# Kernel optimization log

Measured on AMD Instinct MI355X. Metric: run time of the kernel, lower is better.

## Reference

```python
import jax, jax.numpy as jnp
import numpy as np

SIGMA = 1.0
ALPHA = 1.5
EPS = 1e-08
N, D = 8192, 128


def setup_inputs() -> dict:
    key = jax.random.key(0)
    k1, k2 = jax.random.split(key)
    z1 = jax.random.normal(k1, (N, D), dtype=jnp.float32)
    z2 = jax.random.normal(k2, (N, D), dtype=jnp.float32)
    return {"z1": z1, "z2": z2}


def _l2_normalize(x, eps=1e-12):
    # matches F.normalize(x, dim=1): x / max(||x||, eps)
    n = jnp.linalg.norm(x, axis=1, keepdims=True)
    return x / jnp.maximum(n, eps)


def _f_prime(u):
    # KL divergence: f'(u) = log(u + eps) + 1
    return jnp.log(u + EPS) + 1.0


def _f_star(t):
    # KL divergence conjugate: f*(t) = exp(t - 1)
    return jnp.exp(t - 1.0)


def reference(z1, z2):
    z1 = _l2_normalize(z1)
    z2 = _l2_normalize(z2)
    n = z1.shape[0]

    # positive term: ||z1_i - z2_i||^2 per row
    d_pos = jnp.sum((z1 - z2) ** 2, axis=1)                       # (N,)
    g_pos = jnp.exp(-d_pos / (2.0 * SIGMA ** 2))
    s_pos = _f_prime(g_pos)

    # negative term: squared pairwise distances within z1 (N x N)
    sq = jnp.sum(z1 * z1, axis=1)                                  # (N,)
    d2 = sq[:, None] + sq[None, :] - 2.0 * (z1 @ z1.T)             # (N, N)
    d2 = jnp.maximum(d2, 0.0)
    g_neg = jnp.exp(-d2 / (2.0 * SIGMA ** 2))
    s_neg = _f_prime(g_neg)
    star_neg = _f_star(s_neg)

    # masked mean over off-diagonal entries (N*(N-1) of them)
    off_diag = 1.0 - jnp.eye(n, dtype=star_neg.dtype)
    star_mean = jnp.sum(star_neg * off_diag) / (n * (n - 1))

    loss = -jnp.mean(s_pos) + ALPHA * star_mean
    return loss
```

## Files before the change

### kernel.cpp

```cpp
#include <hip/hip_runtime.h>

#define NROWS 8192
#define DIM 128
#define NT 64
#define NPAIRBLK (NT * (NT + 1) / 2)
#define NNORMBLK 2048

typedef _Float16 f16x8 __attribute__((ext_vector_type(8)));
typedef float f32x16 __attribute__((ext_vector_type(16)));

__global__ void fmicl_normalize(const float* __restrict__ z1,
                                const float* __restrict__ z2,
                                float* __restrict__ sq,
                                _Float16* __restrict__ zh,
                                float* __restrict__ spos) {
  const int row = blockIdx.x * 4 + (threadIdx.x >> 6);
  const int lane = threadIdx.x & 63;
  const float* r1 = z1 + (size_t)row * DIM;
  const float* r2 = z2 + (size_t)row * DIM;
  float a0 = r1[lane], a1 = r1[lane + 64];
  float b0 = r2[lane], b1 = r2[lane + 64];
  float s1 = a0 * a0 + a1 * a1;
  float s2 = b0 * b0 + b1 * b1;
#pragma unroll
  for (int off = 32; off; off >>= 1) {
    s1 += __shfl_xor(s1, off);
    s2 += __shfl_xor(s2, off);
  }
  const float inv1 = 1.0f / fmaxf(sqrtf(s1), 1e-12f);
  const float inv2 = 1.0f / fmaxf(sqrtf(s2), 1e-12f);
  const float n1a = a0 * inv1, n1b = a1 * inv1;
  const float n2a = b0 * inv2, n2b = b1 * inv2;
  float sqp = n1a * n1a + n1b * n1b;
  const float da = n1a - n2a, db = n1b - n2b;
  float dp = da * da + db * db;
#pragma unroll
  for (int off = 32; off; off >>= 1) {
    sqp += __shfl_xor(sqp, off);
    dp += __shfl_xor(dp, off);
  }
  zh[(size_t)row * DIM + lane] = (_Float16)n1a;
  zh[(size_t)row * DIM + lane + 64] = (_Float16)n1b;
  if (lane == 0) {
    sq[row] = sqp;
    spos[row] = logf(expf(-0.5f * dp) + 1e-8f) + 1.0f;
  }
}

__global__ __launch_bounds__(512, 4) void fmicl_pairwise(
    const _Float16* __restrict__ zh,
    const float* __restrict__ sq,
    float* __restrict__ pairP) {
  __shared__ _Float16 As[128 * DIM];
  __shared__ _Float16 Bs[128 * DIM];
  __shared__ float wsum[8];

  const int tid = threadIdx.x;
  const int bid = blockIdx.x;

  int rt = (int)(64.5f - sqrtf(64.5f * 64.5f - 2.0f * (float)bid));
  if (rt < 0) rt = 0;
  while (rt > 0 && (rt * NT - (rt * (rt - 1)) / 2) > bid) --rt;
  while (((rt + 1) * NT - ((rt + 1) * rt) / 2) <= bid) ++rt;
  const int ct = rt + (bid - (rt * NT - (rt * (rt - 1)) / 2));

  const int lane = tid & 63;
  const int wid = tid >> 6;
  const int i0 = rt << 7;
  const int j0 = ct << 7;

  const uint4* __restrict__ gA = (const uint4*)(zh + (size_t)i0 * DIM);
  const uint4* __restrict__ gB = (const uint4*)(zh + (size_t)j0 * DIM);
  uint4* sA = (uint4*)As;
  uint4* sB = (uint4*)Bs;
#pragma unroll
  for (int it = 0; it < 4; ++it) {
    const int g = tid + it * 512;
    const int r = g >> 4;
    const int c = g & 15;
    const uint4 va = gA[g];
    const uint4 vb = gB[g];
    const int cs = c ^ (r & 15);
    sA[r * 16 + cs] = va;
    sB[r * 16 + cs] = vb;
  }
  __syncthreads();

  const int l31 = lane & 31;
  const int lhi = lane >> 5;
  const int wm = (wid >> 2) * 64;
  const int wn = (wid & 3) * 32;

  const int ra0 = wm + l31;
  const int ra1 = wm + 32 + l31;
  const int rb = wn + l31;
  f32x16 acc0 = {}, acc1 = {};
#pragma unroll
  for (int ks = 0; ks < 8; ++ks) {
    const int kg = ks * 2 + lhi;
    const uint4 va0 = sA[ra0 * 16 + (kg ^ (ra0 & 15))];
    const uint4 va1 = sA[ra1 * 16 + (kg ^ (ra1 & 15))];
    const uint4 vb = sB[rb * 16 + (kg ^ (rb & 15))];
    const f16x8 bfr = __builtin_bit_cast(f16x8, vb);
    acc0 = __builtin_amdgcn_mfma_f32_32x32x16_f16(
        __builtin_bit_cast(f16x8, va0), bfr, acc0, 0, 0, 0);
    acc1 = __builtin_amdgcn_mfma_f32_32x32x16_f16(
        __builtin_bit_cast(f16x8, va1), bfr, acc1, 0, 0, 0);
  }

  const int gj = j0 + wn + l31;
  const float sj = sq[gj];
  float gsum = 0.0f;
#pragma unroll
  for (int mi = 0; mi < 2; ++mi) {
    const f32x16& acc = mi ? acc1 : acc0;
    const int mbase = wm + mi * 32;
    float4 sqi_q[4];
#pragma unroll
    for (int q = 0; q < 4; ++q)
      sqi_q[q] = *(const float4*)&sq[i0 + mbase + 4 * lhi + 8 * q];
#pragma unroll
    for (int r = 0; r < 16; ++r) {
      const int mloc = (r & 3) + 4 * lhi + 8 * (r >> 2);
      const float si = ((const float*)&sqi_q[r >> 2])[r & 3];
      const float d2 = fmaxf(si + sj - 2.0f * acc[r], 0.0f);
      const float gg = __expf(-0.5f * d2);
      gsum += ((i0 + mbase + mloc) != gj) ? gg : 0.0f;
    }
  }
#pragma unroll
  for (int off = 32; off; off >>= 1) gsum += __shfl_xor(gsum, off);
  if (lane == 0) wsum[wid] = gsum;
  __syncthreads();
  if (tid == 0) {
    const float w = (rt == ct) ? 1.0f : 2.0f;
    float s = 0.0f;
#pragma unroll
    for (int k = 0; k < 8; ++k) s += wsum[k];
    pairP[bid] = w * s;
  }
}

__global__ void fmicl_reduce(const float* __restrict__ pairP,
                             const float* __restrict__ spos,
                             float* __restrict__ out) {
  const int t = threadIdx.x;
  double nsum = (double)pairP[t] + (double)pairP[t + 1024];
  if (t < NPAIRBLK - 2048) nsum += (double)pairP[t + 2048];
  double psum = 0.0;
#pragma unroll
  for (int k = 0; k < 8; ++k) psum += (double)spos[t + 1024 * k];
#pragma unroll
  for (int off = 32; off; off >>= 1) {
    nsum += __shfl_xor(nsum, off);
    psum += __shfl_xor(psum, off);
  }
  __shared__ double ls[2][16];
  const int lane = t & 63;
  const int wid = t >> 6;
  if (lane == 0) {
    ls[0][wid] = nsum;
    ls[1][wid] = psum;
  }
  __syncthreads();
  if (t == 0) {
    double n = 0.0, p = 0.0;
#pragma unroll
    for (int k = 0; k < 16; ++k) {
      n += ls[0][k];
      p += ls[1][k];
    }
    const double pos_mean = p / (double)NROWS;
    const double star_mean = n / ((double)NROWS * (double)(NROWS - 1)) + 1e-8;
    out[0] = (float)(-pos_mean + 1.5 * star_mean);
  }
}

extern "C" void kernel_launch(void* const* d_in, const int* in_sizes, int n_in,
                              void* d_out, int out_size, void* d_ws,
                              size_t ws_size, hipStream_t stream) {
  const float* z1 = (const float*)d_in[0];
  const float* z2 = (const float*)d_in[1];
  float* out = (float*)d_out;
  char* ws = (char*)d_ws;

  float* pairP = (float*)(ws + 0);
  float* spos = (float*)(ws + 16384);
  float* sq = (float*)(ws + 49152);
  _Float16* zh = (_Float16*)(ws + 81920);

  fmicl_normalize<<<NNORMBLK, 256, 0, stream>>>(z1, z2, sq, zh, spos);
  fmicl_pairwise<<<NPAIRBLK, 512, 0, stream>>>(zh, sq, pairP);
  fmicl_reduce<<<1, 1024, 0, stream>>>(pairP, spos, out);
}
```

Baseline: 33.73 us.

## Fuse final reduction into pairwise kernel via last-block atomic ticket

Removes the separate reduce kernel launch: the last pairwise block, found with an atomic counter, does the final double-precision reduction. Normalize pre-reduces the positive term per block and resets the counter. The pairwise kernel moves to 1024 threads with one MFMA tile per wave, loads global memory straight into LDS with global_load_lds, and uses exp2 with folded constants, skipping the diagonal mask except on diagonal warps. This trades a launch and some ALU work for atomic/fence overhead and the removal of the d2 clamp, which can slightly change numerics.

```diff
diff --git a/kernel.cpp b/kernel.cpp
--- a/kernel.cpp
+++ b/kernel.cpp
@@ -4,24 +4,28 @@
 #define DIM 128
 #define NT 64
 #define NPAIRBLK (NT * (NT + 1) / 2)
-#define NNORMBLK 2048
 
 typedef _Float16 f16x8 __attribute__((ext_vector_type(8)));
+typedef _Float16 f16x2 __attribute__((ext_vector_type(2)));
 typedef float f32x16 __attribute__((ext_vector_type(16)));
 
-__global__ void fmicl_normalize(const float* __restrict__ z1,
-                                const float* __restrict__ z2,
-                                float* __restrict__ sq,
-                                _Float16* __restrict__ zh,
-                                float* __restrict__ spos) {
-  const int row = blockIdx.x * 4 + (threadIdx.x >> 6);
+#define KHL2E 0.7213475204444817f
+#define L2E 1.4426950408889634f
+
+#define AS1(p) ((const __attribute__((address_space(1))) void*)(p))
+#define AS3(p) ((__attribute__((address_space(3))) void*)(p))
+
+__global__ __launch_bounds__(1024) void fmicl_normalize(
+    const float* __restrict__ z1, const float* __restrict__ z2,
+    float* __restrict__ sq, _Float16* __restrict__ zh,
+    float* __restrict__ sposB, unsigned int* __restrict__ counter) {
+  const int wid = threadIdx.x >> 6;
   const int lane = threadIdx.x & 63;
-  const float* r1 = z1 + (size_t)row * DIM;
-  const float* r2 = z2 + (size_t)row * DIM;
-  float a0 = r1[lane], a1 = r1[lane + 64];
-  float b0 = r2[lane], b1 = r2[lane + 64];
-  float s1 = a0 * a0 + a1 * a1;
-  float s2 = b0 * b0 + b1 * b1;
+  const int row = blockIdx.x * 16 + wid;
+  const float2 a = ((const float2*)(z1 + (size_t)row * DIM))[lane];
+  const float2 b = ((const float2*)(z2 + (size_t)row * DIM))[lane];
+  float s1 = a.x * a.x + a.y * a.y;
+  float s2 = b.x * b.x + b.y * b.y;
 #pragma unroll
   for (int off = 32; off; off >>= 1) {
     s1 += __shfl_xor(s1, off);
@@ -29,31 +33,43 @@
   }
   const float inv1 = 1.0f / fmaxf(sqrtf(s1), 1e-12f);
   const float inv2 = 1.0f / fmaxf(sqrtf(s2), 1e-12f);
-  const float n1a = a0 * inv1, n1b = a1 * inv1;
-  const float n2a = b0 * inv2, n2b = b1 * inv2;
-  float sqp = n1a * n1a + n1b * n1b;
-  const float da = n1a - n2a, db = n1b - n2b;
-  float dp = da * da + db * db;
+  const float n1x = a.x * inv1, n1y = a.y * inv1;
+  const float n2x = b.x * inv2, n2y = b.y * inv2;
+  float sqp = n1x * n1x + n1y * n1y;
+  const float dx = n1x - n2x, dy = n1y - n2y;
+  float dp = dx * dx + dy * dy;
 #pragma unroll
   for (int off = 32; off; off >>= 1) {
     sqp += __shfl_xor(sqp, off);
     dp += __shfl_xor(dp, off);
   }
-  zh[(size_t)row * DIM + lane] = (_Float16)n1a;
-  zh[(size_t)row * DIM + lane + 64] = (_Float16)n1b;
+  f16x2 h;
+  h.x = (_Float16)n1x;
+  h.y = (_Float16)n1y;
+  *(f16x2*)(zh + (size_t)row * DIM + 2 * lane) = h;
+  __shared__ float sposL[16];
   if (lane == 0) {
     sq[row] = sqp;
-    spos[row] = logf(expf(-0.5f * dp) + 1e-8f) + 1.0f;
+    sposL[wid] = logf(expf(-0.5f * dp) + 1e-8f) + 1.0f;
+  }
+  __syncthreads();
+  if (threadIdx.x == 0) {
+    float s = 0.0f;
+#pragma unroll
+    for (int k = 0; k < 16; ++k) s += sposL[k];
+    sposB[blockIdx.x] = s;
+    if (blockIdx.x == 0) *counter = 0;
   }
 }
 
-__global__ __launch_bounds__(512, 4) void fmicl_pairwise(
-    const _Float16* __restrict__ zh,
-    const float* __restrict__ sq,
-    float* __restrict__ pairP) {
-  __shared__ _Float16 As[128 * DIM];
-  __shared__ _Float16 Bs[128 * DIM];
-  __shared__ float wsum[8];
+__global__ __launch_bounds__(1024, 8) void fmicl_pairwise(
+    const _Float16* __restrict__ zh, const float* __restrict__ sq,
+    float* __restrict__ pairP, const float* __restrict__ sposB,
+    unsigned int* __restrict__ counter, float* __restrict__ out) {
+  __shared__ _Float16 S[256 * DIM];
+  __shared__ float wsum[16];
+  __shared__ double red[32];
+  __shared__ int amLast;
 
   const int tid = threadIdx.x;
   const int bid = blockIdx.x;
@@ -69,63 +85,59 @@
   const int i0 = rt << 7;
   const int j0 = ct << 7;
 
-  const uint4* __restrict__ gA = (const uint4*)(zh + (size_t)i0 * DIM);
-  const uint4* __restrict__ gB = (const uint4*)(zh + (size_t)j0 * DIM);
-  uint4* sA = (uint4*)As;
-  uint4* sB = (uint4*)Bs;
-#pragma unroll
-  for (int it = 0; it < 4; ++it) {
-    const int g = tid + it * 512;
-    const int r = g >> 4;
-    const int c = g & 15;
-    const uint4 va = gA[g];
-    const uint4 vb = gB[g];
-    const int cs = c ^ (r & 15);
-    sA[r * 16 + cs] = va;
-    sB[r * 16 + cs] = vb;
+#pragma unroll
+  for (int t = 0; t < 4; ++t) {
+    const int P = t * 16 + wid;
+    const int R = P * 4 + (lane >> 4);
+    const int csrc = (lane & 15) ^ (R & 15);
+    const _Float16* srow = (R < 128) ? zh + (size_t)(i0 + R) * DIM
+                                     : zh + (size_t)(j0 + R - 128) * DIM;
+    __builtin_amdgcn_global_load_lds(AS1(srow + csrc * 8), AS3(S + P * 512),
+                                     16, 0, 0);
   }
   __syncthreads();
 
   const int l31 = lane & 31;
   const int lhi = lane >> 5;
-  const int wm = (wid >> 2) * 64;
+  const int wm = (wid >> 2) * 32;
   const int wn = (wid & 3) * 32;
-
-  const int ra0 = wm + l31;
-  const int ra1 = wm + 32 + l31;
-  const int rb = wn + l31;
-  f32x16 acc0 = {}, acc1 = {};
+  const uint4* S4 = (const uint4*)S;
+  const int ra = wm + l31;
+  const int rb = 128 + wn + l31;
+  f32x16 acc = {};
 #pragma unroll
   for (int ks = 0; ks < 8; ++ks) {
     const int kg = ks * 2 + lhi;
-    const uint4 va0 = sA[ra0 * 16 + (kg ^ (ra0 & 15))];
-    const uint4 va1 = sA[ra1 * 16 + (kg ^ (ra1 & 15))];
-    const uint4 vb = sB[rb * 16 + (kg ^ (rb & 15))];
-    const f16x8 bfr = __builtin_bit_cast(f16x8, vb);
-    acc0 = __builtin_amdgcn_mfma_f32_32x32x16_f16(
-        __builtin_bit_cast(f16x8, va0), bfr, acc0, 0, 0, 0);
-    acc1 = __builtin_amdgcn_mfma_f32_32x32x16_f16(
-        __builtin_bit_cast(f16x8, va1), bfr, acc1, 0, 0, 0);
+    const uint4 va = S4[ra * 16 + (kg ^ (ra & 15))];
+    const uint4 vb = S4[rb * 16 + (kg ^ (rb & 15))];
+    acc = __builtin_amdgcn_mfma_f32_32x32x16_f16(
+        __builtin_bit_cast(f16x8, va), __builtin_bit_cast(f16x8, vb), acc,
+        0, 0, 0);
   }
 
   const int gj = j0 + wn + l31;
-  const float sj = sq[gj];
+  const float ksj = KHL2E * sq[gj];
+  float4 sqi[4];
+#pragma unroll
+  for (int q = 0; q < 4; ++q)
+    sqi[q] = *(const float4*)&sq[i0 + wm + 4 * lhi + 8 * q];
   float gsum = 0.0f;
-#pragma unroll
-  for (int mi = 0; mi < 2; ++mi) {
-    const f32x16& acc = mi ? acc1 : acc0;
-    const int mbase = wm + mi * 32;
-    float4 sqi_q[4];
-#pragma unroll
-    for (int q = 0; q < 4; ++q)
-      sqi_q[q] = *(const float4*)&sq[i0 + mbase + 4 * lhi + 8 * q];
+  const bool diagw = (rt == ct) && (wm == wn);
+  if (diagw) {
 #pragma unroll
     for (int r = 0; r < 16; ++r) {
+      const float si = ((const float*)&sqi[r >> 2])[r & 3];
+      const float c = fmaf(KHL2E, si, ksj);
+      const float e = __builtin_amdgcn_exp2f(fmaf(L2E, acc[r], -c));
       const int mloc = (r & 3) + 4 * lhi + 8 * (r >> 2);
-      const float si = ((const float*)&sqi_q[r >> 2])[r & 3];
-      const float d2 = fmaxf(si + sj - 2.0f * acc[r], 0.0f);
-      const float gg = __expf(-0.5f * d2);
-      gsum += ((i0 + mbase + mloc) != gj) ? gg : 0.0f;
+      gsum += (mloc != l31) ? e : 0.0f;
+    }
+  } else {
+#pragma unroll
+    for (int r = 0; r < 16; ++r) {
+      const float si = ((const float*)&sqi[r >> 2])[r & 3];
+      const float c = fmaf(KHL2E, si, ksj);
+      gsum += __builtin_amdgcn_exp2f(fmaf(L2E, acc[r], -c));
     }
   }
 #pragma unroll
@@ -133,46 +145,43 @@
   if (lane == 0) wsum[wid] = gsum;
   __syncthreads();
   if (tid == 0) {
-    const float w = (rt == ct) ? 1.0f : 2.0f;
     float s = 0.0f;
 #pragma unroll
-    for (int k = 0; k < 8; ++k) s += wsum[k];
-    pairP[bid] = w * s;
-  }
-}
-
-__global__ void fmicl_reduce(const float* __restrict__ pairP,
-                             const float* __restrict__ spos,
-                             float* __restrict__ out) {
-  const int t = threadIdx.x;
-  double nsum = (double)pairP[t] + (double)pairP[t + 1024];
-  if (t < NPAIRBLK - 2048) nsum += (double)pairP[t + 2048];
-  double psum = 0.0;
-#pragma unroll
-  for (int k = 0; k < 8; ++k) psum += (double)spos[t + 1024 * k];
-#pragma unroll
-  for (int off = 32; off; off >>= 1) {
-    nsum += __shfl_xor(nsum, off);
-    psum += __shfl_xor(psum, off);
-  }
-  __shared__ double ls[2][16];
-  const int lane = t & 63;
-  const int wid = t >> 6;
-  if (lane == 0) {
-    ls[0][wid] = nsum;
-    ls[1][wid] = psum;
-  }
-  __syncthreads();
-  if (t == 0) {
-    double n = 0.0, p = 0.0;
-#pragma unroll
-    for (int k = 0; k < 16; ++k) {
-      n += ls[0][k];
-      p += ls[1][k];
-    }
-    const double pos_mean = p / (double)NROWS;
-    const double star_mean = n / ((double)NROWS * (double)(NROWS - 1)) + 1e-8;
-    out[0] = (float)(-pos_mean + 1.5 * star_mean);
+    for (int k = 0; k < 16; ++k) s += wsum[k];
+    pairP[bid] = (rt == ct) ? s : 2.0f * s;
+    __threadfence();
+    const unsigned int tkt = atomicAdd(counter, 1u);
+    amLast = (tkt == NPAIRBLK - 1) ? 1 : 0;
+  }
+  __syncthreads();
+
+  if (amLast) {
+    __threadfence();
+    double nsum = (double)pairP[tid] + (double)pairP[tid + 1024];
+    if (tid < NPAIRBLK - 2048) nsum += (double)pairP[tid + 2048];
+    double psum = (tid < 512) ? (double)sposB[tid] : 0.0;
+#pragma unroll
+    for (int off = 32; off; off >>= 1) {
+      nsum += __shfl_xor(nsum, off);
+      psum += __shfl_xor(psum, off);
+    }
+    if (lane == 0) {
+      red[wid] = nsum;
+      red[16 + wid] = psum;
+    }
+    __syncthreads();
+    if (tid == 0) {
+      double n = 0.0, p = 0.0;
+#pragma unroll
+      for (int k = 0; k < 16; ++k) {
+        n += red[k];
+        p += red[16 + k];
+      }
+      const double pos_mean = p / (double)NROWS;
+      const double star_mean =
+          n / ((double)NROWS * (double)(NROWS - 1)) + 1e-8;
+      out[0] = (float)(-pos_mean + 1.5 * star_mean);
+    }
   }
 }
 
@@ -184,12 +193,13 @@
   float* out = (float*)d_out;
   char* ws = (char*)d_ws;
 
-  float* pairP = (float*)(ws + 0);
-  float* spos = (float*)(ws + 16384);
-  float* sq = (float*)(ws + 49152);
-  _Float16* zh = (_Float16*)(ws + 81920);
-
-  fmicl_normalize<<<NNORMBLK, 256, 0, stream>>>(z1, z2, sq, zh, spos);
-  fmicl_pairwise<<<NPAIRBLK, 512, 0, stream>>>(zh, sq, pairP);
-  fmicl_reduce<<<1, 1024, 0, stream>>>(pairP, spos, out);
+  unsigned int* counter = (unsigned int*)ws;
+  float* pairP = (float*)(ws + 64);
+  float* sposB = (float*)(ws + 8448);
+  float* sq = (float*)(ws + 10496);
+  _Float16* zh = (_Float16*)(ws + 43264);
+
+  fmicl_normalize<<<512, 1024, 0, stream>>>(z1, z2, sq, zh, sposB, counter);
+  fmicl_pairwise<<<NPAIRBLK, 1024, 0, stream>>>(zh, sq, pairP, sposB, counter,
+                                                out);
 }
```

After: 66.59 us. 97.4% more time.
